# Optimization experiments

Measured on AMD Instinct MI355X. Metric: run time of the kernel, lower is better.

The kernel has to match this reference:

```python
import jax, jax.numpy as jnp
import numpy as np

E = 1024  # embedding_dim
D = 1024  # output_dim

def setup_inputs() -> dict:
    key = jax.random.key(0)
    k_x, k_q, k_k, k_v = jax.random.split(key, 4)
    embeddings = jax.random.normal(k_x, (4, 2048, E), dtype=jnp.float32)
    scale = 1.0 / np.sqrt(E)
    Wq = jax.random.normal(k_q, (E, D), dtype=jnp.float32) * scale
    Wk = jax.random.normal(k_k, (E, D), dtype=jnp.float32) * scale
    Wv = jax.random.normal(k_v, (E, D), dtype=jnp.float32) * scale
    return {"embeddings": embeddings, "Wq": Wq, "Wk": Wk, "Wv": Wv}

def reference(embeddings, Wq, Wk, Wv):
    # QKV projections (no bias, qkv_bias=False)
    q = jnp.einsum('bse,ed->bsd', embeddings, Wq)
    k = jnp.einsum('bse,ed->bsd', embeddings, Wk)
    v = jnp.einsum('bse,ed->bsd', embeddings, Wv)
    n = embeddings.shape[1]
    scores = jnp.einsum('bqd,bkd->bqk', q, k)  # [B, S, S]
    causal = jnp.tril(jnp.ones((n, n), dtype=bool))  # mask upper triangle (diag=1)
    scores = jnp.where(causal, scores, -jnp.inf)
    scale = jnp.asarray(k.shape[-1], scores.dtype) ** 0.5
    weights = jax.nn.softmax(scores / scale, axis=-1)
    # dropout p=0.0 -> identity
    context = jnp.einsum('bqk,bkd->bqd', weights, v)
    return context
```

## Files before the change

kernel.cpp:

```cpp
#include <hip/hip_runtime.h>
#include <hip/hip_fp16.h>

typedef unsigned short u16;
typedef __attribute__((ext_vector_type(8))) short short8;
typedef __attribute__((ext_vector_type(4))) float f32x4;
typedef __attribute__((ext_vector_type(4))) unsigned short u16x4;
typedef __attribute__((ext_vector_type(4))) float float4v;

__device__ __forceinline__ u16 f2bf(float f) {
  union { float f; unsigned u; } v; v.f = f;
  unsigned r = v.u + 0x7FFFu + ((v.u >> 16) & 1u);
  return (u16)(r >> 16);
}

__device__ __forceinline__ u16 f2h(float f) {
  __half h = __float2half(f);
  return *reinterpret_cast<u16*>(&h);
}

__device__ __forceinline__ float h2f(u16 b) {
  __half_raw hr; hr.x = b;
  return __half2float(__half(hr));
}

__device__ __forceinline__ void gload16(const void* g, void* l) {
  __builtin_amdgcn_global_load_lds(
      (const __attribute__((address_space(1))) unsigned int*)g,
      (__attribute__((address_space(3))) unsigned int*)l, 16, 0, 0);
}

__global__ __launch_bounds__(256) void kconv(const float* __restrict__ X,
                                             const float* __restrict__ Wq,
                                             const float* __restrict__ Wk,
                                             const float* __restrict__ Wv,
                                             u16* __restrict__ Xb,
                                             u16* __restrict__ Wt) {
  __shared__ float tile[32][33];
  const int bx = blockIdx.x;
  if (bx < 8192) {
    size_t i = ((size_t)bx * 256 + threadIdx.x) * 4;
    float4v v = *(const float4v*)(X + i);
    u16x4 o;
    o.x = f2bf(v.x); o.y = f2bf(v.y); o.z = f2bf(v.z); o.w = f2bf(v.w);
    *(u16x4*)(Xb + i) = o;
  } else {
    const int l = bx - 8192;
    const int z = l >> 10;
    const int rem = l & 1023;
    const int n0 = (rem & 31) * 32, k0 = (rem >> 5) * 32;
    const float* W = z == 0 ? Wq : (z == 1 ? Wk : Wv);
    u16* O = Wt + (size_t)z * 1024 * 1024;
    const int tx = threadIdx.x & 31, ty = threadIdx.x >> 5;
#pragma unroll
    for (int r = 0; r < 32; r += 8)
      tile[ty + r][tx] = W[(size_t)(k0 + ty + r) * 1024 + n0 + tx];
    __syncthreads();
#pragma unroll
    for (int r = 0; r < 32; r += 8)
      O[(size_t)(n0 + ty + r) * 1024 + k0 + tx] = f2bf(tile[tx][ty + r]);
  }
}

__device__ __forceinline__ void stage64(const u16* __restrict__ pan, int ld,
                                        int k0, u16* dst, int t) {
  const int rb = t >> 3;
  const int sw = ((t & 7) ^ (rb & 7)) * 8;
  const int ds = (t & 7) * 8;
#pragma unroll
  for (int j = 0; j < 4; ++j) {
    const int row = j * 32 + rb;
    gload16(pan + (size_t)row * ld + k0 + sw, dst + row * 64 + ds);
  }
}

__device__ __forceinline__ void gemm64(const u16* __restrict__ A,
                                       const u16* __restrict__ B,
                                       int lda, int ldb,
                                       int rowBase, int colBase, int kIters,
                                       u16* As, u16* Bs, f32x4 acc[4][4]) {
  const int t = threadIdx.x;
  const int wid = t >> 6, lane = t & 63;
  const int wm = wid >> 1, wn = wid & 1;
  const int l15 = lane & 15;
  const int sw = l15 & 7;
  const int sl = lane >> 4;
  const int s0 = ((sl    ) ^ sw) * 8;
  const int s1 = ((sl + 4) ^ sw) * 8;
  const u16* ga = A + (size_t)rowBase * lda;
  const u16* gb = B + (size_t)colBase * ldb;

  for (int kt = 0; kt < kIters; ++kt) {
    const int k0 = kt * 64;
    stage64(ga, lda, k0, As, t);
    stage64(gb, ldb, k0, Bs, t);
    __syncthreads();
#pragma unroll
    for (int h = 0; h < 2; ++h) {
      const int so = h ? s1 : s0;
      short8 a[4], b[4];
#pragma unroll
      for (int mi = 0; mi < 4; mi++)
        a[mi] = *(const short8*)(As + (wm * 64 + mi * 16 + l15) * 64 + so);
#pragma unroll
      for (int ni = 0; ni < 4; ni++)
        b[ni] = *(const short8*)(Bs + (wn * 64 + ni * 16 + l15) * 64 + so);
#pragma unroll
      for (int mi = 0; mi < 4; mi++)
#pragma unroll
        for (int ni = 0; ni < 4; ni++)
          acc[mi][ni] = __builtin_amdgcn_mfma_f32_16x16x32_bf16(
              a[mi], b[ni], acc[mi][ni], 0, 0, 0);
    }
    __syncthreads();
  }
}

__global__ __launch_bounds__(256, 3) void kqkv(const u16* __restrict__ Xb,
                                               const u16* __restrict__ Wt,
                                               u16* __restrict__ Qb,
                                               u16* __restrict__ Kb,
                                               u16* __restrict__ Vt) {
  __shared__ __align__(16) u16 As[128 * 64];
  __shared__ __align__(16) u16 Bs[128 * 64];
  const f32x4 z4 = {0.f, 0.f, 0.f, 0.f};
  f32x4 acc[4][4];
#pragma unroll
  for (int i = 0; i < 4; i++)
#pragma unroll
    for (int j = 0; j < 4; j++) acc[i][j] = z4;

  const int l = blockIdx.x;
  const int xcd = l & 7, idx = l >> 3;
  const int cz = idx >> 3, rloc = idx & 7;
  const int rowTile = xcd * 8 + rloc;
  const int z = cz >> 3, colTile = cz & 7;

  const int rowBase = rowTile * 128, colBase = colTile * 128;
  const u16* Bt = Wt + (size_t)z * 1024 * 1024;
  gemm64(Xb, Bt, 1024, 1024, rowBase, colBase, 16, As, Bs, acc);

  const int t = threadIdx.x, wid = t >> 6, lane = t & 63;
  const int wm = wid >> 1, wn = wid & 1;
  const int r0 = rowBase + wm * 64 + ((lane >> 4) * 4);
  const int c0 = colBase + wn * 64 + (lane & 15);
  if (z < 2) {
    u16* O = z ? Kb : Qb;
#pragma unroll
    for (int mi = 0; mi < 4; mi++) {
      int r = r0 + mi * 16;
#pragma unroll
      for (int ni = 0; ni < 4; ni++) {
        int c = c0 + ni * 16;
#pragma unroll
        for (int j = 0; j < 4; j++)
          O[(size_t)(r + j) * 1024 + c] = f2bf(acc[mi][ni][j]);
      }
    }
  } else {
#pragma unroll
    for (int mi = 0; mi < 4; mi++) {
      int s0r = r0 + mi * 16;
      int bb = s0r >> 11, sl = s0r & 2047;
#pragma unroll
      for (int ni = 0; ni < 4; ni++) {
        int d = c0 + ni * 16;
        u16x4 pk;
        pk.x = f2bf(acc[mi][ni][0]);
        pk.y = f2bf(acc[mi][ni][1]);
        pk.z = f2bf(acc[mi][ni][2]);
        pk.w = f2bf(acc[mi][ni][3]);
        *(u16x4*)(Vt + ((size_t)bb * 1024 + d) * 2048 + sl) = pk;
      }
    }
  }
}

__global__ __launch_bounds__(256, 3) void kscores(const u16* __restrict__ Q,
                                                  const u16* __restrict__ K,
                                                  u16* __restrict__ Sch) {
  const int x = blockIdx.x, b = blockIdx.y;
  const int xcd = x & 7, idx = x >> 3;
  const int tid = xcd * 17 + idx;
  int tr = (int)((sqrtf(8.f * tid + 1.f) - 1.f) * 0.5f);
  while ((tr + 1) * (tr + 2) / 2 <= tid) ++tr;
  while (tr * (tr + 1) / 2 > tid) --tr;
  const int tc = tid - tr * (tr + 1) / 2;

  __shared__ __align__(16) u16 As[128 * 64];
  __shared__ __align__(16) u16 Bs[128 * 64];
  const f32x4 z4 = {0.f, 0.f, 0.f, 0.f};
  f32x4 acc[4][4];
#pragma unroll
  for (int i = 0; i < 4; i++)
#pragma unroll
    for (int j = 0; j < 4; j++) acc[i][j] = z4;

  const u16* Qp = Q + (size_t)b * 2048 * 1024;
  const u16* Kp = K + (size_t)b * 2048 * 1024;
  gemm64(Qp, Kp, 1024, 1024, tr * 128, tc * 128, 16, As, Bs, acc);

  u16* S = Sch + (size_t)b * 2048 * 2048;
  const int t = threadIdx.x, wid = t >> 6, lane = t & 63;
  const int wm = wid >> 1, wn = wid & 1;
  const int r0 = tr * 128 + wm * 64 + ((lane >> 4) * 4);
  const int c0 = tc * 128 + wn * 64 + (lane & 15);
#pragma unroll
  for (int mi = 0; mi < 4; mi++) {
    int r = r0 + mi * 16;
#pragma unroll
    for (int ni = 0; ni < 4; ni++) {
      int c = c0 + ni * 16;
#pragma unroll
      for (int j = 0; j < 4; j++)
        S[(size_t)(r + j) * 2048 + c] = f2h(acc[mi][ni][j] * 0.03125f);
    }
  }
}

__global__ __launch_bounds__(256) void ksoftmax(const u16* __restrict__ Sch,
                                                u16* __restrict__ P) {
  const int i = blockIdx.x, b = blockIdx.y;
  const int t = threadIdx.x, lane = t & 63, wid = t >> 6;
  const int nceil = ((i >> 7) + 1) << 7;
  __shared__ float red[4];

  const size_t rowoff = ((size_t)b * 2048 + i) * 2048 + t * 8;
  const int base = t * 8;
  short8 raw = {0, 0, 0, 0, 0, 0, 0, 0};
  if (base < nceil) raw = *(const short8*)(Sch + rowoff);
  float v[8];
#pragma unroll
  for (int k = 0; k < 8; ++k)
    v[k] = (base + k <= i) ? h2f((u16)raw[k]) : -3.0e38f;

  float lm = v[0];
#pragma unroll
  for (int k = 1; k < 8; ++k) lm = fmaxf(lm, v[k]);
#pragma unroll
  for (int o = 32; o > 0; o >>= 1) lm = fmaxf(lm, __shfl_down(lm, o));
  if (lane == 0) red[wid] = lm;
  __syncthreads();
  const float m = fmaxf(fmaxf(red[0], red[1]), fmaxf(red[2], red[3]));
  __syncthreads();

  float e[8], ls = 0.f;
#pragma unroll
  for (int k = 0; k < 8; ++k) {
    e[k] = __expf(fmaxf(v[k] - m, -88.f));
    ls += e[k];
  }
#pragma unroll
  for (int o = 32; o > 0; o >>= 1) ls += __shfl_down(ls, o);
  if (lane == 0) red[wid] = ls;
  __syncthreads();
  const float inv = 1.f / (red[0] + red[1] + red[2] + red[3]);

  if (base < nceil) {
    short8 out;
#pragma unroll
    for (int k = 0; k < 8; ++k) out[k] = (short)f2bf(e[k] * inv);
    *(short8*)(P + rowoff) = out;
  }
}

__global__ __launch_bounds__(256, 3) void kpv(const u16* __restrict__ P,
                                              const u16* __restrict__ Vt,
                                              float* __restrict__ Out) {
  const int x = blockIdx.x, b = blockIdx.y;
  const int xcd = x & 7, idx = x >> 3;
  const int tr = (idx & 1) ? (15 - xcd) : xcd;
  const int col = idx >> 1;

  __shared__ __align__(16) u16 As[128 * 64];
  __shared__ __align__(16) u16 Bs[128 * 64];
  const f32x4 z4 = {0.f, 0.f, 0.f, 0.f};
  f32x4 acc[4][4];
#pragma unroll
  for (int i = 0; i < 4; i++)
#pragma unroll
    for (int j = 0; j < 4; j++) acc[i][j] = z4;

  const u16* Pp = P + (size_t)b * 2048 * 2048;
  const u16* Vp = Vt + (size_t)b * 1024 * 2048;
  gemm64(Pp, Vp, 2048, 2048, tr * 128, col * 128, (tr + 1) * 2, As, Bs, acc);

  float* Ob = Out + (size_t)b * 2048 * 1024;
  const int t = threadIdx.x, wid = t >> 6, lane = t & 63;
  const int wm = wid >> 1, wn = wid & 1;
  const int r0 = tr * 128 + wm * 64 + ((lane >> 4) * 4);
  const int c0 = col * 128 + wn * 64 + (lane & 15);
#pragma unroll
  for (int mi = 0; mi < 4; mi++) {
    int r = r0 + mi * 16;
#pragma unroll
    for (int ni = 0; ni < 4; ni++) {
      int c = c0 + ni * 16;
#pragma unroll
      for (int j = 0; j < 4; j++)
        Ob[(size_t)(r + j) * 1024 + c] = acc[mi][ni][j];
    }
  }
}

extern "C" void kernel_launch(void* const* d_in, const int* in_sizes, int n_in,
                              void* d_out, int out_size, void* d_ws,
                              size_t ws_size, hipStream_t stream) {
  const float* X = (const float*)d_in[0];
  const float* Wq = (const float*)d_in[1];
  const float* Wk = (const float*)d_in[2];
  const float* Wv = (const float*)d_in[3];
  float* Out = (float*)d_out;

  char* ws = (char*)d_ws;
  u16* Xb = (u16*)(ws);
  u16* Wt = (u16*)(ws + 16777216);
  u16* Qb = (u16*)(ws + 23068672);
  u16* Kb = (u16*)(ws + 39845888);
  u16* Vt = (u16*)(ws + 56623104);
  u16* Sch = (u16*)(ws + 73400320);
  u16* P = (u16*)(ws + 140509184);

  kconv<<<11264, 256, 0, stream>>>(X, Wq, Wk, Wv, Xb, Wt);
  kqkv<<<1536, 256, 0, stream>>>(Xb, Wt, Qb, Kb, Vt);
  kscores<<<dim3(136, 4), 256, 0, stream>>>(Qb, Kb, Sch);
  ksoftmax<<<dim3(2048, 4), 256, 0, stream>>>(Sch, P);
  kpv<<<dim3(128, 4), 256, 0, stream>>>(P, Vt, Out);
}
```

Before: 139.2 us.

## Fold Wq·Wk^T into one matrix and drop the K projection

The scores are rewritten as X·(Wq·Wk^T)·X^T. A new small kernel computes the 1024x1024 product Wq·Wk^T in bf16 with the 1/sqrt(D) scale folded in. The QKV kernel then computes only X·M and V, and the scores GEMM uses the bf16 embeddings directly as the key side. This removes one third of the projection GEMM work and the K buffer. In exchange it adds a serial low-occupancy GEMM launch (64 blocks) and an extra bf16 rounding of the combined matrix, which may shift accuracy.

```diff
diff --git a/kernel.cpp b/kernel.cpp
--- a/kernel.cpp
+++ b/kernel.cpp
@@ -34,7 +34,9 @@
                                              const float* __restrict__ Wk,
                                              const float* __restrict__ Wv,
                                              u16* __restrict__ Xb,
-                                             u16* __restrict__ Wt) {
+                                             u16* __restrict__ Wqb,
+                                             u16* __restrict__ Wkb,
+                                             u16* __restrict__ Wvt) {
   __shared__ float tile[32][33];
   const int bx = blockIdx.x;
   if (bx < 8192) {
@@ -43,21 +45,26 @@
     u16x4 o;
     o.x = f2bf(v.x); o.y = f2bf(v.y); o.z = f2bf(v.z); o.w = f2bf(v.w);
     *(u16x4*)(Xb + i) = o;
+  } else if (bx < 9216) {
+    const int rem = bx - 8192;
+    const int n0 = (rem & 31) * 32, k0 = (rem >> 5) * 32;
+    const int tx = threadIdx.x & 31, ty = threadIdx.x >> 5;
+#pragma unroll
+    for (int r = 0; r < 32; r += 8)
+      tile[ty + r][tx] = Wv[(size_t)(k0 + ty + r) * 1024 + n0 + tx];
+    __syncthreads();
+#pragma unroll
+    for (int r = 0; r < 32; r += 8)
+      Wvt[(size_t)(n0 + ty + r) * 1024 + k0 + tx] = f2bf(tile[tx][ty + r]);
   } else {
-    const int l = bx - 8192;
-    const int z = l >> 10;
-    const int rem = l & 1023;
-    const int n0 = (rem & 31) * 32, k0 = (rem >> 5) * 32;
-    const float* W = z == 0 ? Wq : (z == 1 ? Wk : Wv);
-    u16* O = Wt + (size_t)z * 1024 * 1024;
-    const int tx = threadIdx.x & 31, ty = threadIdx.x >> 5;
-#pragma unroll
-    for (int r = 0; r < 32; r += 8)
-      tile[ty + r][tx] = W[(size_t)(k0 + ty + r) * 1024 + n0 + tx];
-    __syncthreads();
-#pragma unroll
-    for (int r = 0; r < 32; r += 8)
-      O[(size_t)(n0 + ty + r) * 1024 + k0 + tx] = f2bf(tile[tx][ty + r]);
+    const int l = bx - 9216;
+    const float* W = (l < 1024) ? Wq : Wk;
+    u16* O = (l < 1024) ? Wqb : Wkb;
+    size_t i = ((size_t)(l & 1023) * 256 + threadIdx.x) * 4;
+    float4v v = *(const float4v*)(W + i);
+    u16x4 o;
+    o.x = f2bf(v.x); o.y = f2bf(v.y); o.z = f2bf(v.z); o.w = f2bf(v.w);
+    *(u16x4*)(O + i) = o;
   }
 }
 
@@ -115,10 +122,42 @@
   }
 }
 
+__global__ __launch_bounds__(256, 3) void kmul(const u16* __restrict__ Wkb,
+                                               const u16* __restrict__ Wqb,
+                                               u16* __restrict__ Mt) {
+  __shared__ __align__(16) u16 As[128 * 64];
+  __shared__ __align__(16) u16 Bs[128 * 64];
+  const f32x4 z4 = {0.f, 0.f, 0.f, 0.f};
+  f32x4 acc[4][4];
+#pragma unroll
+  for (int i = 0; i < 4; i++)
+#pragma unroll
+    for (int j = 0; j < 4; j++) acc[i][j] = z4;
+
+  const int rowBase = (blockIdx.x >> 3) * 128, colBase = (blockIdx.x & 7) * 128;
+  gemm64(Wkb, Wqb, 1024, 1024, rowBase, colBase, 16, As, Bs, acc);
+
+  const int t = threadIdx.x, wid = t >> 6, lane = t & 63;
+  const int wm = wid >> 1, wn = wid & 1;
+  const int r0 = rowBase + wm * 64 + ((lane >> 4) * 4);
+  const int c0 = colBase + wn * 64 + (lane & 15);
+#pragma unroll
+  for (int mi = 0; mi < 4; mi++) {
+    int r = r0 + mi * 16;
+#pragma unroll
+    for (int ni = 0; ni < 4; ni++) {
+      int c = c0 + ni * 16;
+#pragma unroll
+      for (int j = 0; j < 4; j++)
+        Mt[(size_t)(r + j) * 1024 + c] = f2bf(acc[mi][ni][j] * 0.03125f);
+    }
+  }
+}
+
 __global__ __launch_bounds__(256, 3) void kqkv(const u16* __restrict__ Xb,
-                                               const u16* __restrict__ Wt,
+                                               const u16* __restrict__ Mt,
+                                               const u16* __restrict__ Wvt,
                                                u16* __restrict__ Qb,
-                                               u16* __restrict__ Kb,
                                                u16* __restrict__ Vt) {
   __shared__ __align__(16) u16 As[128 * 64];
   __shared__ __align__(16) u16 Bs[128 * 64];
@@ -136,15 +175,14 @@
   const int z = cz >> 3, colTile = cz & 7;
 
   const int rowBase = rowTile * 128, colBase = colTile * 128;
-  const u16* Bt = Wt + (size_t)z * 1024 * 1024;
+  const u16* Bt = z ? Wvt : Mt;
   gemm64(Xb, Bt, 1024, 1024, rowBase, colBase, 16, As, Bs, acc);
 
   const int t = threadIdx.x, wid = t >> 6, lane = t & 63;
   const int wm = wid >> 1, wn = wid & 1;
   const int r0 = rowBase + wm * 64 + ((lane >> 4) * 4);
   const int c0 = colBase + wn * 64 + (lane & 15);
-  if (z < 2) {
-    u16* O = z ? Kb : Qb;
+  if (z == 0) {
 #pragma unroll
     for (int mi = 0; mi < 4; mi++) {
       int r = r0 + mi * 16;
@@ -153,7 +191,7 @@
         int c = c0 + ni * 16;
 #pragma unroll
         for (int j = 0; j < 4; j++)
-          O[(size_t)(r + j) * 1024 + c] = f2bf(acc[mi][ni][j]);
+          Qb[(size_t)(r + j) * 1024 + c] = f2bf(acc[mi][ni][j]);
       }
     }
   } else {
@@ -176,7 +214,7 @@
 }
 
 __global__ __launch_bounds__(256, 3) void kscores(const u16* __restrict__ Q,
-                                                  const u16* __restrict__ K,
+                                                  const u16* __restrict__ Xb,
                                                   u16* __restrict__ Sch) {
   const int x = blockIdx.x, b = blockIdx.y;
   const int xcd = x & 7, idx = x >> 3;
@@ -196,7 +234,7 @@
     for (int j = 0; j < 4; j++) acc[i][j] = z4;
 
   const u16* Qp = Q + (size_t)b * 2048 * 1024;
-  const u16* Kp = K + (size_t)b * 2048 * 1024;
+  const u16* Kp = Xb + (size_t)b * 2048 * 1024;
   gemm64(Qp, Kp, 1024, 1024, tr * 128, tc * 128, 16, As, Bs, acc);
 
   u16* S = Sch + (size_t)b * 2048 * 2048;
@@ -212,7 +250,7 @@
       int c = c0 + ni * 16;
 #pragma unroll
       for (int j = 0; j < 4; j++)
-        S[(size_t)(r + j) * 2048 + c] = f2h(acc[mi][ni][j] * 0.03125f);
+        S[(size_t)(r + j) * 2048 + c] = f2h(acc[mi][ni][j]);
     }
   }
 }
@@ -312,17 +350,20 @@
   float* Out = (float*)d_out;
 
   char* ws = (char*)d_ws;
-  u16* Xb = (u16*)(ws);
-  u16* Wt = (u16*)(ws + 16777216);
-  u16* Qb = (u16*)(ws + 23068672);
-  u16* Kb = (u16*)(ws + 39845888);
-  u16* Vt = (u16*)(ws + 56623104);
-  u16* Sch = (u16*)(ws + 73400320);
-  u16* P = (u16*)(ws + 140509184);
-
-  kconv<<<11264, 256, 0, stream>>>(X, Wq, Wk, Wv, Xb, Wt);
-  kqkv<<<1536, 256, 0, stream>>>(Xb, Wt, Qb, Kb, Vt);
-  kscores<<<dim3(136, 4), 256, 0, stream>>>(Qb, Kb, Sch);
+  u16* Xb  = (u16*)(ws);
+  u16* Wqb = (u16*)(ws + 16777216);
+  u16* Wkb = (u16*)(ws + 18874368);
+  u16* Wvt = (u16*)(ws + 20971520);
+  u16* Mt  = (u16*)(ws + 23068672);
+  u16* Qb  = (u16*)(ws + 25165824);
+  u16* Vt  = (u16*)(ws + 41943040);
+  u16* Sch = (u16*)(ws + 58720256);
+  u16* P   = (u16*)(ws + 92274688);
+
+  kconv<<<11264, 256, 0, stream>>>(X, Wq, Wk, Wv, Xb, Wqb, Wkb, Wvt);
+  kmul<<<64, 256, 0, stream>>>(Wkb, Wqb, Mt);
+  kqkv<<<1024, 256, 0, stream>>>(Xb, Mt, Wvt, Qb, Vt);
+  kscores<<<dim3(136, 4), 256, 0, stream>>>(Qb, Xb, Sch);
   ksoftmax<<<dim3(2048, 4), 256, 0, stream>>>(Sch, P);
   kpv<<<dim3(128, 4), 256, 0, stream>>>(P, Vt, Out);
 }
```

Measured after the change: 147.3 us. +5.8%, slower.
